# Kernel tuning notes

Measured on AMD Instinct MI355X. Metric: run time of the kernel, lower is better.

## Reference

```python
import jax, jax.numpy as jnp
import numpy as np

B, LQ, LD, H, DIM, PF = 16, 64, 2048, 1024, 128, 4
MAXK = LD // PF + 1  # static upper bound on num clusters (valid_len <= LD)


def setup_inputs() -> dict:
    key = jax.random.key(0)
    k1, k2, k3, k4 = jax.random.split(key, 4)
    return {
        "q_hidden": jax.random.normal(k1, (B, LQ, H), jnp.float32),
        "d_hidden": jax.random.normal(k2, (B, LD, H), jnp.float32),
        "W": jax.random.normal(k3, (H, DIM), jnp.float32) * (1.0 / np.sqrt(H)),  # xavier-ish
        "b": jnp.zeros((DIM,), jnp.float32),
        "q_mask": jnp.ones((B, LQ), jnp.int32),
        "d_mask": jnp.ones((B, LD), jnp.int32),
        "labels": jax.random.randint(k4, (B, LD), 0, MAXK, dtype=jnp.int32),
        "pooling_factor": PF,
    }


def _encode(hidden, W, b, mask):
    # proj -> L2 normalize -> zero out padded tokens
    r = hidden @ W + b
    r = r / jnp.clip(jnp.linalg.norm(r, axis=-1, keepdims=True), 1e-12)
    return r * mask[..., None].astype(r.dtype)


def _pool(d_repr, d_mask, labels, pf):
    # segment-mean per batch sample, cluster labels supplied externally
    Bn, L, D = d_repr.shape
    max_k = L // pf + 1  # static
    valid = jnp.clip(d_mask.sum(-1), 2, None)          # [B]
    k = valid // pf + 1                                 # per-sample num clusters
    lab = jnp.where(d_mask > 0, labels % k[:, None], max_k)  # invalid tokens -> dummy seg
    seg = lambda vals, idx: jax.ops.segment_sum(vals, idx, num_segments=max_k + 1)
    sums = jax.vmap(seg)(d_repr, lab)[:, :max_k]                          # [B,K,D]
    counts = jax.vmap(seg)(jnp.where(d_mask > 0, 1.0, 0.0), lab)[:, :max_k]
    means = sums / jnp.clip(counts, 1.0)[..., None]
    means = means / jnp.clip(jnp.linalg.norm(means, axis=-1, keepdims=True), 1e-12)
    pad_mask = jnp.arange(max_k)[None, :] < k[:, None]                    # [B,K]
    return means * pad_mask[..., None], pad_mask


def reference(q_hidden, d_hidden, W, b, q_mask, d_mask, labels, pooling_factor):
    q = _encode(q_hidden, W, b, q_mask)            # [B,LQ,DIM]
    d = _encode(d_hidden, W, b, d_mask)            # [B,LD,DIM]
    d_pool, pmask = _pool(d, d_mask, labels, pooling_factor)  # [B,K,DIM]
    sim = jnp.einsum('bqd,bkd->bqk', q, d_pool)
    sim = jnp.where(pmask[:, None, :], sim, -1e4)
    score = (sim.max(-1) * q_mask.astype(sim.dtype)).sum(-1)  # maxsum per pair
    return score
```

## Files before the change

kernel.cpp:

```cpp
#include <hip/hip_runtime.h>
#include <hip/hip_bf16.h>

#define BB    16
#define LQ    64
#define LD    2048
#define HH    1024
#define DIM   128
#define MAXK  513
#define SCH   9

typedef __attribute__((ext_vector_type(8))) short short8;
typedef __attribute__((ext_vector_type(4))) float f32x4;

__device__ __forceinline__ float b2f(ushort u) {
    union { float f; unsigned int u32; } c; c.u32 = ((unsigned int)u) << 16; return c.f;
}
__device__ __forceinline__ ushort f2b_rn(float f) {
    unsigned int x = __float_as_uint(f);
    return (ushort)((x + 0x7fffu + ((x >> 16) & 1u)) >> 16);
}

__device__ __forceinline__ void gld16(void* lds, const void* g) {
    __builtin_amdgcn_global_load_lds(
        (const __attribute__((address_space(1))) unsigned int*)g,
        (__attribute__((address_space(3))) unsigned int*)lds,
        16, 0, 0);
}

__global__ __launch_bounds__(256) void prep_kb_kernel(
    const float* __restrict__ W,
    const int*   __restrict__ d_mask,
    const int*   __restrict__ pf,
    ushort*      __restrict__ Wt,
    int*         __restrict__ kvals,
    float*       __restrict__ sums)
{
    int bid = blockIdx.x, t = threadIdx.x;
    if (bid < 16) {
        __shared__ ushort tile[128][72];
        const int h0 = bid * 64;
        #pragma unroll
        for (int i = 0; i < 32; ++i) {
            int flat = i * 256 + t;
            int r = flat >> 7, c = flat & 127;
            tile[c][r] = f2b_rn(W[(long)(h0 + r) * DIM + c]);
        }
        __syncthreads();
        #pragma unroll
        for (int i = 0; i < 4; ++i) {
            int flat = i * 256 + t;
            int n = flat >> 3, u = flat & 7;
            uint4 v = *(const uint4*)&tile[n][u * 8];
            *(uint4*)&Wt[(long)n * HH + h0 + u * 8] = v;
        }
    } else if (bid < 32) {
        __shared__ int red[4];
        int b = bid - 16;
        int lane = t & 63, wave = t >> 6;
        int s = 0;
        for (int i = t; i < LD; i += 256) s += (d_mask[b * LD + i] > 0) ? 1 : 0;
        #pragma unroll
        for (int m = 1; m < 64; m <<= 1) s += __shfl_xor(s, m);
        if (lane == 0) red[wave] = s;
        __syncthreads();
        if (t == 0) {
            int v = red[0] + red[1] + red[2] + red[3];
            if (v < 2) v = 2;
            int pfv = pf[0];
            if (pfv < 1 || pfv > LD) pfv = 4;
            kvals[b] = v / pfv + 1;
        }
    } else {
        const int total4 = (BB * MAXK * DIM) / 4;
        float4* s4 = (float4*)sums;
        const float4 z = make_float4(0.f, 0.f, 0.f, 0.f);
        for (int i = (bid - 32) * 256 + t; i < total4; i += 256 * 256)
            s4[i] = z;
    }
}

__global__ __launch_bounds__(256, 2) void encode_kernel(
    const float*  __restrict__ X,
    const ushort* __restrict__ Wt,
    const float*  __restrict__ bias,
    const int*    __restrict__ mask,
    const int*    __restrict__ labels,
    const int*    __restrict__ kvals,
    float*        __restrict__ sums,
    float*        __restrict__ q_repr,
    int           isq)
{
    __shared__ __align__(16) uint4 lds[4096];

    const int t = threadIdx.x;
    const int w = t >> 6, lane = t & 63;
    const int m16 = lane & 15, quad = lane >> 4;

    const int unit = blockIdx.x * 4 + w;
    const long row0 = (long)unit * 16;

    f32x4 acc[8];
    #pragma unroll
    for (int j = 0; j < 8; ++j) acc[j] = (f32x4){0.f, 0.f, 0.f, 0.f};

    const int sw8 = m16 & 7;

    const float* gA = X + (row0 + (lane >> 3)) * HH
                        + (((lane & 7) ^ ((lane >> 3) & 7)) * 4);

    auto stage = [&](int b, int hp) {
        const int bofs = b * 2048;
        #pragma unroll
        for (int i = 0; i < 4; ++i) {
            int Si = w * 256 + i * 64 + lane;
            int n = Si >> 3, up = Si & 7;
            const ushort* src = Wt + (long)n * HH + (hp * 8 + (up ^ (n & 7))) * 8;
            gld16(&lds[bofs + w * 256 + i * 64], src);
        }
        #pragma unroll
        for (int s = 0; s < 2; ++s) {
            const long ko = (long)(hp * 2 + s) * 32;
            gld16(&lds[bofs + 1024 + w * 256 + s * 128], gA + ko);
            gld16(&lds[bofs + 1024 + w * 256 + s * 128 + 64], gA + 8 * HH + ko);
        }
    };

    auto compute = [&](int b) {
        const ushort* Wu = (const ushort*)&lds[b * 2048];
        const float4* Af = (const float4*)&lds[b * 2048 + 1024 + w * 256];
        #pragma unroll
        for (int cc = 0; cc < 2; ++cc) {
            float4 va0 = Af[cc * 128 + m16 * 8 + ((2 * quad) ^ sw8)];
            float4 va1 = Af[cc * 128 + m16 * 8 + ((2 * quad + 1) ^ sw8)];
            float av[8];
            *(float4*)(av)     = va0;
            *(float4*)(av + 4) = va1;
            short8 ah;
            #pragma unroll
            for (int j = 0; j < 8; ++j) ah[j] = (short)f2b_rn(av[j]);
            #pragma unroll
            for (int ct = 0; ct < 8; ++ct) {
                short8 bf = *(const short8*)
                    &Wu[((ct * 16 + m16) * 8 + ((cc * 4 + quad) ^ sw8)) * 8];
                acc[ct] = __builtin_amdgcn_mfma_f32_16x16x32_bf16(ah, bf, acc[ct], 0, 0, 0);
            }
        }
    };

    stage(0, 0);
    stage(1, 1);

    for (int i = 0; i < 15; ++i) {
        asm volatile("s_waitcnt vmcnt(8)" ::: "memory");
        __builtin_amdgcn_s_barrier();
        __builtin_amdgcn_sched_barrier(0);
        compute(i & 1);
        __builtin_amdgcn_s_barrier();
        __builtin_amdgcn_sched_barrier(0);
        if (i + 2 < 16) stage(i & 1, i + 2);
    }
    asm volatile("s_waitcnt vmcnt(0)" ::: "memory");
    __builtin_amdgcn_s_barrier();
    __builtin_amdgcn_sched_barrier(0);
    compute(1);

    float bia[8];
    #pragma unroll
    for (int ct = 0; ct < 8; ++ct) bia[ct] = bias[ct * 16 + m16];

    float vv[8][4];
    float ssp[4] = {0.f, 0.f, 0.f, 0.f};
    #pragma unroll
    for (int ct = 0; ct < 8; ++ct)
        #pragma unroll
        for (int r = 0; r < 4; ++r) {
            vv[ct][r] = acc[ct][r] + bia[ct];
            ssp[r] += vv[ct][r] * vv[ct][r];
        }
    #pragma unroll
    for (int r = 0; r < 4; ++r) {
        ssp[r] += __shfl_xor(ssp[r], 1);
        ssp[r] += __shfl_xor(ssp[r], 2);
        ssp[r] += __shfl_xor(ssp[r], 4);
        ssp[r] += __shfl_xor(ssp[r], 8);
    }

    #pragma unroll
    for (int r = 0; r < 4; ++r) {
        long rowg = row0 + quad * 4 + r;
        float scale = 1.0f / fmaxf(sqrtf(ssp[r]), 1e-12f);
        if (isq) {
            scale *= (float)mask[rowg];
            #pragma unroll
            for (int ct = 0; ct < 8; ++ct)
                q_repr[rowg * DIM + ct * 16 + m16] = vv[ct][r] * scale;
        } else if (mask[rowg] > 0) {
            int b = (int)(rowg >> 11);
            int seg = labels[rowg] % kvals[b];
            float* sp = sums + ((long)b * MAXK + seg) * DIM + m16;
            #pragma unroll
            for (int ct = 0; ct < 8; ++ct)
                atomicAdd(sp + ct * 16, vv[ct][r] * scale);
        }
    }
}

__global__ __launch_bounds__(256) void simmax_kernel(
    const float* __restrict__ q_repr,
    const float* __restrict__ sums,
    const int*   __restrict__ kvals,
    float*       __restrict__ pmax)
{
    __shared__ __align__(16) ushort Qh[64 * 136];
    __shared__ __align__(16) ushort Ql[64 * 136];
    __shared__ __align__(16) ushort Ch[64 * 136];
    __shared__ float cn[64];

    int b = blockIdx.x / SCH, chunk = blockIdx.x % SCH;
    int t = threadIdx.x, w = t >> 6, lane = t & 63;
    int m16 = lane & 15, quad = lane >> 4;

    #pragma unroll
    for (int i = 0; i < 8; ++i) {
        int flat = i * 256 + t;
        int row = flat >> 5, c4 = flat & 31;
        float4 v = *(const float4*)(q_repr + ((long)b * LQ + row) * DIM + c4 * 4);
        float x[4]; *(float4*)x = v;
        ushort4 h, l;
        ushort* hp = (ushort*)&h; ushort* lp = (ushort*)&l;
        #pragma unroll
        for (int j = 0; j < 4; ++j) {
            unsigned int ux = __float_as_uint(x[j]);
            hp[j] = (ushort)(ux >> 16);
            lp[j] = f2b_rn(x[j] - __uint_as_float(ux & 0xffff0000u));
        }
        *(ushort4*)&Qh[row * 136 + c4 * 4] = h;
        *(ushort4*)&Ql[row * 136 + c4 * 4] = l;
    }
    #pragma unroll
    for (int i = 0; i < 8; ++i) {
        int flat = i * 256 + t;
        int row = flat >> 5, c4 = flat & 31;
        int kk = chunk * 64 + row;
        float4 v = (kk < MAXK)
            ? *(const float4*)(sums + ((long)b * MAXK + kk) * DIM + c4 * 4)
            : make_float4(0.f, 0.f, 0.f, 0.f);
        ushort4 h; ushort* hp = (ushort*)&h;
        hp[0] = f2b_rn(v.x); hp[1] = f2b_rn(v.y);
        hp[2] = f2b_rn(v.z); hp[3] = f2b_rn(v.w);
        *(ushort4*)&Ch[row * 136 + c4 * 4] = h;
    }
    __syncthreads();

    {
        int c = w * 16 + m16;
        float ssv = 0.f;
        #pragma unroll
        for (int j = 0; j < 16; ++j) {
            unsigned int u = *(const unsigned int*)&Ch[c * 136 + quad * 32 + j * 2];
            float x0 = b2f((ushort)u), x1 = b2f((ushort)(u >> 16));
            ssv += x0 * x0 + x1 * x1;
        }
        ssv += __shfl_xor(ssv, 16);
        ssv += __shfl_xor(ssv, 32);
        if (quad == 0) cn[c] = (ssv > 1e-24f) ? rsqrtf(ssv) : 0.f;
    }
    __syncthreads();

    f32x4 acc[4];
    #pragma unroll
    for (int j = 0; j < 4; ++j) acc[j] = (f32x4){0.f, 0.f, 0.f, 0.f};

    #pragma unroll
    for (int kc = 0; kc < 4; ++kc) {
        short8 qh = *(const short8*)&Qh[(w * 16 + m16) * 136 + kc * 32 + quad * 8];
        short8 ql = *(const short8*)&Ql[(w * 16 + m16) * 136 + kc * 32 + quad * 8];
        #pragma unroll
        for (int ct = 0; ct < 4; ++ct) {
            short8 cf = *(const short8*)&Ch[(ct * 16 + m16) * 136 + kc * 32 + quad * 8];
            acc[ct] = __builtin_amdgcn_mfma_f32_16x16x32_bf16(qh, cf, acc[ct], 0, 0, 0);
            acc[ct] = __builtin_amdgcn_mfma_f32_16x16x32_bf16(ql, cf, acc[ct], 0, 0, 0);
        }
    }

    int kb = kvals[b];
    #pragma unroll
    for (int r = 0; r < 4; ++r) {
        float mx = -1e4f;
        #pragma unroll
        for (int ct = 0; ct < 4; ++ct) {
            int cl = chunk * 64 + ct * 16 + m16;
            float sim = acc[ct][r] * cn[ct * 16 + m16];
            mx = fmaxf(mx, (cl < kb) ? sim : -1e4f);
        }
        mx = fmaxf(mx, __shfl_xor(mx, 1));
        mx = fmaxf(mx, __shfl_xor(mx, 2));
        mx = fmaxf(mx, __shfl_xor(mx, 4));
        mx = fmaxf(mx, __shfl_xor(mx, 8));
        if (m16 == 0)
            pmax[((long)b * SCH + chunk) * 64 + w * 16 + quad * 4 + r] = mx;
    }
}

__global__ __launch_bounds__(64) void final_kernel(
    const float* __restrict__ pmax,
    const int*   __restrict__ q_mask,
    float*       __restrict__ out)
{
    int b = blockIdx.x, r = threadIdx.x;
    float m = -3e38f;
    #pragma unroll
    for (int c = 0; c < SCH; ++c)
        m = fmaxf(m, pmax[((long)b * SCH + c) * 64 + r]);
    m *= (float)q_mask[b * LQ + r];
    #pragma unroll
    for (int sh = 1; sh < 64; sh <<= 1) m += __shfl_xor(m, sh);
    if (r == 0) out[b] = m;
}

extern "C" void kernel_launch(void* const* d_in, const int* in_sizes, int n_in,
                              void* d_out, int out_size, void* d_ws, size_t ws_size,
                              hipStream_t stream) {
    const float* q_hidden = (const float*)d_in[0];
    const float* d_hidden = (const float*)d_in[1];
    const float* W        = (const float*)d_in[2];
    const float* bias     = (const float*)d_in[3];
    const int*   q_mask   = (const int*)d_in[4];
    const int*   d_mask   = (const int*)d_in[5];
    const int*   labels   = (const int*)d_in[6];
    const int*   pf       = (const int*)d_in[7];

    float* ws     = (float*)d_ws;
    float* q_repr = ws;
    float* sums   = q_repr + (long)BB * LQ * DIM;
    float* pmaxb  = sums + (long)BB * MAXK * DIM;
    int*   kvals  = (int*)(pmaxb + BB * SCH * 64);
    ushort* Wt    = (ushort*)(kvals + 16);

    prep_kb_kernel<<<288, 256, 0, stream>>>(W, d_mask, pf, Wt, kvals, sums);
    encode_kernel<<<16, 256, 0, stream>>>(q_hidden, Wt, bias, q_mask,
                                          labels, kvals, sums, q_repr, 1);
    encode_kernel<<<512, 256, 0, stream>>>(d_hidden, Wt, bias, d_mask,
                                           labels, kvals, sums, q_repr, 0);
    simmax_kernel<<<BB * SCH, 256, 0, stream>>>(q_repr, sums, kvals, pmaxb);
    final_kernel<<<BB, 64, 0, stream>>>(pmaxb, q_mask, (float*)d_out);
}
```

Measured before the change: 257.9 us.

## Split-K encode across two wave groups and merge q/d encode launches

```diff
diff --git a/kernel.cpp b/kernel.cpp
--- a/kernel.cpp
+++ b/kernel.cpp
@@ -79,25 +79,33 @@
     }
 }
 
-__global__ __launch_bounds__(256, 2) void encode_kernel(
-    const float*  __restrict__ X,
+__global__ __launch_bounds__(512, 4) void encode_kernel(
+    const float*  __restrict__ Xd,
+    const float*  __restrict__ Xq,
     const ushort* __restrict__ Wt,
     const float*  __restrict__ bias,
-    const int*    __restrict__ mask,
+    const int*    __restrict__ mask_d,
+    const int*    __restrict__ mask_q,
     const int*    __restrict__ labels,
     const int*    __restrict__ kvals,
     float*        __restrict__ sums,
-    float*        __restrict__ q_repr,
-    int           isq)
+    float*        __restrict__ q_repr)
 {
     __shared__ __align__(16) uint4 lds[4096];
 
-    const int t = threadIdx.x;
+    const int bid = blockIdx.x, t = threadIdx.x;
     const int w = t >> 6, lane = t & 63;
     const int m16 = lane & 15, quad = lane >> 4;
-
-    const int unit = blockIdx.x * 4 + w;
-    const long row0 = (long)unit * 16;
+    const int g = w >> 2;
+    const int ui = w & 3;
+
+    const int unit = (bid < 512) ? (bid * 4 + ui) : (2048 + (bid - 512) * 4 + ui);
+    const bool isq = unit >= 2048;
+    const long row0 = isq ? (long)(unit - 2048) * 16 : (long)unit * 16;
+    const float* Xb = isq ? Xq : Xd;
+
+    const float* gA = Xb + (row0 + (lane >> 3)) * HH
+                         + (((lane & 7) ^ ((lane >> 3) & 7)) * 4);
 
     f32x4 acc[8];
     #pragma unroll
@@ -105,45 +113,40 @@
 
     const int sw8 = m16 & 7;
 
-    const float* gA = X + (row0 + (lane >> 3)) * HH
-                        + (((lane & 7) ^ ((lane >> 3) & 7)) * 4);
-
-    auto stage = [&](int b, int hp) {
+    auto stage = [&](int b, int it) {
         const int bofs = b * 2048;
         #pragma unroll
-        for (int i = 0; i < 4; ++i) {
-            int Si = w * 256 + i * 64 + lane;
-            int n = Si >> 3, up = Si & 7;
-            const ushort* src = Wt + (long)n * HH + (hp * 8 + (up ^ (n & 7))) * 8;
-            gld16(&lds[bofs + w * 256 + i * 64], src);
-        }
-        #pragma unroll
-        for (int s = 0; s < 2; ++s) {
-            const long ko = (long)(hp * 2 + s) * 32;
-            gld16(&lds[bofs + 1024 + w * 256 + s * 128], gA + ko);
-            gld16(&lds[bofs + 1024 + w * 256 + s * 128 + 64], gA + 8 * HH + ko);
-        }
+        for (int i2 = 0; i2 < 2; ++i2) {
+            int Si = w * 128 + i2 * 64 + lane;
+            int gp = Si >> 9;
+            int n  = (Si >> 2) & 127;
+            int up = Si & 3;
+            const ushort* src = Wt + (long)n * HH
+                              + (gp * 512 + it * 32 + (up ^ (n & 3)) * 8);
+            gld16(&lds[bofs + w * 128 + i2 * 64], src);
+        }
+        const long koff = (long)(g * 512 + it * 32);
+        gld16(&lds[bofs + 1024 + w * 128], gA + koff);
+        gld16(&lds[bofs + 1024 + w * 128 + 64], gA + 8 * HH + koff);
     };
 
     auto compute = [&](int b) {
         const ushort* Wu = (const ushort*)&lds[b * 2048];
-        const float4* Af = (const float4*)&lds[b * 2048 + 1024 + w * 256];
-        #pragma unroll
-        for (int cc = 0; cc < 2; ++cc) {
-            float4 va0 = Af[cc * 128 + m16 * 8 + ((2 * quad) ^ sw8)];
-            float4 va1 = Af[cc * 128 + m16 * 8 + ((2 * quad + 1) ^ sw8)];
-            float av[8];
-            *(float4*)(av)     = va0;
-            *(float4*)(av + 4) = va1;
-            short8 ah;
-            #pragma unroll
-            for (int j = 0; j < 8; ++j) ah[j] = (short)f2b_rn(av[j]);
-            #pragma unroll
-            for (int ct = 0; ct < 8; ++ct) {
-                short8 bf = *(const short8*)
-                    &Wu[((ct * 16 + m16) * 8 + ((cc * 4 + quad) ^ sw8)) * 8];
-                acc[ct] = __builtin_amdgcn_mfma_f32_16x16x32_bf16(ah, bf, acc[ct], 0, 0, 0);
-            }
+        const float4* Af = (const float4*)&lds[b * 2048 + 1024 + w * 128];
+        float4 va0 = Af[m16 * 8 + ((2 * quad) ^ sw8)];
+        float4 va1 = Af[m16 * 8 + ((2 * quad + 1) ^ sw8)];
+        float av[8];
+        *(float4*)(av)     = va0;
+        *(float4*)(av + 4) = va1;
+        short8 ah;
+        #pragma unroll
+        for (int j = 0; j < 8; ++j) ah[j] = (short)f2b_rn(av[j]);
+        #pragma unroll
+        for (int ct = 0; ct < 8; ++ct) {
+            const int r = ct * 16 + m16;
+            const int u4 = g * 512 + r * 4 + (quad ^ (r & 3));
+            short8 bf = *(const short8*)&Wu[u4 * 8];
+            acc[ct] = __builtin_amdgcn_mfma_f32_16x16x32_bf16(ah, bf, acc[ct], 0, 0, 0);
         }
     };
 
@@ -151,7 +154,7 @@
     stage(1, 1);
 
     for (int i = 0; i < 15; ++i) {
-        asm volatile("s_waitcnt vmcnt(8)" ::: "memory");
+        asm volatile("s_waitcnt vmcnt(4)" ::: "memory");
         __builtin_amdgcn_s_barrier();
         __builtin_amdgcn_sched_barrier(0);
         compute(i & 1);
@@ -164,43 +167,58 @@
     __builtin_amdgcn_sched_barrier(0);
     compute(1);
 
-    float bia[8];
-    #pragma unroll
-    for (int ct = 0; ct < 8; ++ct) bia[ct] = bias[ct * 16 + m16];
-
-    float vv[8][4];
-    float ssp[4] = {0.f, 0.f, 0.f, 0.f};
-    #pragma unroll
-    for (int ct = 0; ct < 8; ++ct)
+    __syncthreads();
+    if (g == 1) {
+        #pragma unroll
+        for (int j = 0; j < 8; ++j)
+            lds[(w - 4) * 512 + j * 64 + lane] = *(const uint4*)&acc[j];
+    }
+    __syncthreads();
+    if (g == 0) {
+        #pragma unroll
+        for (int j = 0; j < 8; ++j) {
+            f32x4 p = *(const f32x4*)&lds[w * 512 + j * 64 + lane];
+            acc[j] += p;
+        }
+
+        float bia[8];
+        #pragma unroll
+        for (int ct = 0; ct < 8; ++ct) bia[ct] = bias[ct * 16 + m16];
+
+        float vv[8][4];
+        float ssp[4] = {0.f, 0.f, 0.f, 0.f};
+        #pragma unroll
+        for (int ct = 0; ct < 8; ++ct)
+            #pragma unroll
+            for (int r = 0; r < 4; ++r) {
+                vv[ct][r] = acc[ct][r] + bia[ct];
+                ssp[r] += vv[ct][r] * vv[ct][r];
+            }
         #pragma unroll
         for (int r = 0; r < 4; ++r) {
-            vv[ct][r] = acc[ct][r] + bia[ct];
-            ssp[r] += vv[ct][r] * vv[ct][r];
-        }
-    #pragma unroll
-    for (int r = 0; r < 4; ++r) {
-        ssp[r] += __shfl_xor(ssp[r], 1);
-        ssp[r] += __shfl_xor(ssp[r], 2);
-        ssp[r] += __shfl_xor(ssp[r], 4);
-        ssp[r] += __shfl_xor(ssp[r], 8);
-    }
-
-    #pragma unroll
-    for (int r = 0; r < 4; ++r) {
-        long rowg = row0 + quad * 4 + r;
-        float scale = 1.0f / fmaxf(sqrtf(ssp[r]), 1e-12f);
-        if (isq) {
-            scale *= (float)mask[rowg];
-            #pragma unroll
-            for (int ct = 0; ct < 8; ++ct)
-                q_repr[rowg * DIM + ct * 16 + m16] = vv[ct][r] * scale;
-        } else if (mask[rowg] > 0) {
-            int b = (int)(rowg >> 11);
-            int seg = labels[rowg] % kvals[b];
-            float* sp = sums + ((long)b * MAXK + seg) * DIM + m16;
-            #pragma unroll
-            for (int ct = 0; ct < 8; ++ct)
-                atomicAdd(sp + ct * 16, vv[ct][r] * scale);
+            ssp[r] += __shfl_xor(ssp[r], 1);
+            ssp[r] += __shfl_xor(ssp[r], 2);
+            ssp[r] += __shfl_xor(ssp[r], 4);
+            ssp[r] += __shfl_xor(ssp[r], 8);
+        }
+
+        #pragma unroll
+        for (int r = 0; r < 4; ++r) {
+            long rowg = row0 + quad * 4 + r;
+            float scale = 1.0f / fmaxf(sqrtf(ssp[r]), 1e-12f);
+            if (isq) {
+                scale *= (float)mask_q[rowg];
+                #pragma unroll
+                for (int ct = 0; ct < 8; ++ct)
+                    q_repr[rowg * DIM + ct * 16 + m16] = vv[ct][r] * scale;
+            } else if (mask_d[rowg] > 0) {
+                int b = (int)(rowg >> 11);
+                int seg = labels[rowg] % kvals[b];
+                float* sp = sums + ((long)b * MAXK + seg) * DIM + m16;
+                #pragma unroll
+                for (int ct = 0; ct < 8; ++ct)
+                    atomicAdd(sp + ct * 16, vv[ct][r] * scale);
+            }
         }
     }
 }
@@ -338,10 +356,9 @@
     ushort* Wt    = (ushort*)(kvals + 16);
 
     prep_kb_kernel<<<288, 256, 0, stream>>>(W, d_mask, pf, Wt, kvals, sums);
-    encode_kernel<<<16, 256, 0, stream>>>(q_hidden, Wt, bias, q_mask,
-                                          labels, kvals, sums, q_repr, 1);
-    encode_kernel<<<512, 256, 0, stream>>>(d_hidden, Wt, bias, d_mask,
-                                           labels, kvals, sums, q_repr, 0);
+    encode_kernel<<<528, 512, 0, stream>>>(d_hidden, q_hidden, Wt, bias,
+                                           d_mask, q_mask, labels, kvals,
+                                           sums, q_repr);
     simmax_kernel<<<BB * SCH, 256, 0, stream>>>(q_repr, sums, kvals, pmaxb);
     final_kernel<<<BB, 64, 0, stream>>>(pmaxb, q_mask, (float*)d_out);
 }
```

Measured after the change: 248.8 us. -3.5%, faster.
